# Kernel tuning notes

Hardware: AMD Instinct MI355X
Metric: run time of the kernel (lower is better)

Reference implementation:

```python
import jax, jax.numpy as jnp
import numpy as np

# --- GLIF3 / AlphaPSC constants (from NeuronParam / NetworkConfig) ---
N = 2048            # n_neuron
NE = int(N * 0.8)   # excitatory count = 1638
NUM_IN_NEU = 1024
NUM_OUT_NEU = 128
T, B, NUM_IN, NUM_OUT = 100, 64, 784, 10
V_TH, V_RESET = -45.0, -60.0
C_M, TAU = 2.0, 20.0
K_ASC, ASC_AMP = 1.0 / 80.0, -0.2
TAU_REF, BASE_I = 2.0, 0.12
DT = 1.0


def _spike(x):
    # heaviside spike (Erf surrogate only matters for backward)
    return (x >= 0).astype(x.dtype)


def setup_inputs() -> dict:
    key = jax.random.key(0)
    k1, k2, k3, k4 = jax.random.split(key, 4)
    x = jax.random.normal(k1, (T, B, NUM_IN), jnp.float32)
    W_in = jax.random.normal(k2, (NUM_IN_NEU, NUM_IN), jnp.float32) / np.sqrt(NUM_IN)
    W_rec = jax.random.normal(k3, (N, N), jnp.float32) * (5.0 / np.sqrt(N))  # rec_weight_scaling
    W_out = jax.random.normal(k4, (NUM_OUT, NUM_OUT_NEU), jnp.float32) / np.sqrt(NUM_OUT_NEU)
    # replicate NetworkConfig.__post_init__ index sampling (same RandomState, same order)
    rand = np.random.RandomState(32)
    input_indices = jnp.asarray(rand.choice(NE, NUM_IN_NEU, replace=False), jnp.int32)
    output_indices = jnp.asarray(rand.choice(NE, NUM_OUT_NEU, replace=False), jnp.int32)
    tau_syn = jnp.concatenate([jnp.full((NE,), 5.8, jnp.float32),
                               jnp.full((N - NE,), 6.5, jnp.float32)])
    return dict(x=x, W_in=W_in, W_rec=W_rec, W_out=W_out, tau_syn=tau_syn,
                input_indices=input_indices, output_indices=output_indices)


def _run(x, W_in, W_rec, W_out, tau_syn, input_indices, output_indices, spike_fn):
    Tn, Bn, _ = x.shape
    # input projection then scatter into the excitatory input subset
    proj = jnp.einsum('tbi,ni->tbn', x, W_in)                   # (T, B, num_input_neuron)
    inp = jnp.zeros((Tn, Bn, N), x.dtype).at[..., input_indices].set(proj)
    d_syn = jnp.exp(-DT / tau_syn)                              # (N,) per-neuron alpha decay
    e_tau = jnp.e / tau_syn                                     # alpha-kernel peak normalization
    d_asc = jnp.exp(-K_ASC * DT)

    def step(carry, inp_t):
        v, psc, rise, asc, ref, spk = carry
        # recurrent connection + external drive feeds the alpha synapse
        I_in = spk @ W_rec.T + inp_t                            # (B, N)
        psc_n = d_syn * (psc + DT * rise)                       # alpha-PSC (dual-exp) update
        rise_n = d_syn * rise + e_tau * I_in
        asc_n = d_asc * asc + ASC_AMP * spk                     # after-spike current
        active = (ref <= 0).astype(v.dtype)                     # refractory gate
        dv = (psc_n + asc_n + BASE_I) / C_M - (v - V_RESET) / TAU
        v_n = v + active * DT * dv
        spk_n = spike_fn(v_n - V_TH) * active
        v_n = v_n - spk_n * (V_TH - V_RESET)                    # soft reset (hard_reset=False)
        ref_n = jnp.where(spk_n > 0, TAU_REF, jnp.maximum(ref - DT, 0.0))
        return (v_n, psc_n, rise_n, asc_n, ref_n, spk_n), spk_n

    z = jnp.zeros((Bn, N), x.dtype)
    c0 = (jnp.full((Bn, N), V_RESET, x.dtype), z, z, z, z, z)
    _, spikes = jax.lax.scan(step, c0, inp)                     # spikes: (T, B, N)
    rate = spikes[..., output_indices].mean(axis=0)             # (B, num_output_neuron)
    return rate @ W_out.T                                       # (B, num_output)


def reference(x, W_in, W_rec, W_out, tau_syn, input_indices, output_indices):
    return _run(x, W_in, W_rec, W_out, tau_syn, input_indices, output_indices, _spike)
```

## Files before the change

### kernel.cpp

```cpp
#include <hip/hip_runtime.h>
#include <math.h>

#define N_NEU    2048
#define BB       64
#define TT       100
#define KIN      784
#define NIN_NEU  1024
#define N_OUT    10
#define NOUT_NEU 128

typedef unsigned int u32;
typedef unsigned long long u64;
typedef unsigned short u16;

__global__ void k_prep(const float* __restrict__ tau, double* __restrict__ d_syn,
                       double* __restrict__ e_tau){
    int n = blockIdx.x * blockDim.x + threadIdx.x;
    if(n < N_NEU){
        double tv = (double)tau[n];
        d_syn[n] = exp(-1.0 / tv);
        e_tau[n] = 2.718281828459045 / tv;
    }
}

__global__ void k_zero(double* __restrict__ p, long nels, u64* __restrict__ exch, int nexch){
    long i = (long)blockIdx.x * blockDim.x + threadIdx.x;
    long stride = (long)gridDim.x * blockDim.x;
    for(; i < nels; i += stride) p[i] = 0.0;
    int j = blockIdx.x * blockDim.x + threadIdx.x;
    if(j < nexch) exch[j] = 0ull;
}

__global__ __launch_bounds__(256) void k_tr(const float* __restrict__ Wrec, float* __restrict__ Wt){
    __shared__ float tile[32][33];
    int bx = blockIdx.x, by = blockIdx.y;
    int txx = threadIdx.x, tyy = threadIdx.y;
    #pragma unroll
    for(int j=0;j<4;j++)
        tile[tyy+8*j][txx] = Wrec[(size_t)(by*32 + tyy+8*j)*N_NEU + bx*32 + txx];
    __syncthreads();
    #pragma unroll
    for(int j=0;j<4;j++)
        Wt[(size_t)(bx*32 + tyy+8*j)*N_NEU + by*32 + txx] = tile[txx][tyy+8*j];
}

__global__ __launch_bounds__(256) void k_proj(const float* __restrict__ X, const float* __restrict__ Win,
                                              const int* __restrict__ iidx, double* __restrict__ projG){
    __shared__ float As[32][68];
    __shared__ float Bs[32][68];
    const int r0 = blockIdx.x * 64;
    const int c0 = blockIdx.y * 64;
    const int t  = threadIdx.x;
    const int lr = t >> 2;
    const int lk = (t & 3) * 8;
    const int tx = t & 15, ty = t >> 4;
    double acc[4][4] = {};
    for(int k0 = 0; k0 < KIN; k0 += 32){
        int kk = k0 + lk;
        float a8[8], b8[8];
        if(kk + 8 <= KIN){
            const float* pa = X   + (size_t)(r0+lr)*KIN + kk;
            const float* pb = Win + (size_t)(c0+lr)*KIN + kk;
            float4 ra0 = *reinterpret_cast<const float4*>(pa);
            float4 ra1 = *reinterpret_cast<const float4*>(pa + 4);
            float4 rb0 = *reinterpret_cast<const float4*>(pb);
            float4 rb1 = *reinterpret_cast<const float4*>(pb + 4);
            a8[0]=ra0.x; a8[1]=ra0.y; a8[2]=ra0.z; a8[3]=ra0.w;
            a8[4]=ra1.x; a8[5]=ra1.y; a8[6]=ra1.z; a8[7]=ra1.w;
            b8[0]=rb0.x; b8[1]=rb0.y; b8[2]=rb0.z; b8[3]=rb0.w;
            b8[4]=rb1.x; b8[5]=rb1.y; b8[6]=rb1.z; b8[7]=rb1.w;
        } else {
            #pragma unroll
            for(int e=0;e<8;e++){ a8[e]=0.0f; b8[e]=0.0f; }
        }
        #pragma unroll
        for(int e=0;e<8;e++){ As[lk+e][lr] = a8[e]; Bs[lk+e][lr] = b8[e]; }
        __syncthreads();
        #pragma unroll
        for(int kkk=0;kkk<32;kkk++){
            float4 af = *reinterpret_cast<const float4*>(&As[kkk][ty*4]);
            float4 bf = *reinterpret_cast<const float4*>(&Bs[kkk][tx*4]);
            double a[4] = {(double)af.x,(double)af.y,(double)af.z,(double)af.w};
            double b[4] = {(double)bf.x,(double)bf.y,(double)bf.z,(double)bf.w};
            #pragma unroll
            for(int i=0;i<4;i++)
                #pragma unroll
                for(int j=0;j<4;j++)
                    acc[i][j] += a[i]*b[j];
        }
        __syncthreads();
    }
    const int tt = blockIdx.x;
    #pragma unroll
    for(int j=0;j<4;j++){
        int c = c0 + tx*4 + j;
        int n = iidx[c];
        #pragma unroll
        for(int i=0;i<4;i++){
            int b = ty*4 + i;
            projG[((size_t)b*TT + tt)*N_NEU + n] = acc[i][j];
        }
    }
}

__global__ __launch_bounds__(512) void k_sim(
        const double* __restrict__ projG, const float* __restrict__ Wt,
        const double* __restrict__ dsyn, const double* __restrict__ etau,
        u64* __restrict__ exch, double* __restrict__ cntout){
    __shared__ double Ip[4][512];
    __shared__ u32 words[64];
    __shared__ u16 list[N_NEU];
    __shared__ int cntS;

    const int bid = blockIdx.x;
    const int b   = bid >> 2;
    const int q   = bid & 3;
    const int tid = threadIdx.x;
    const int n   = q*512 + tid;
    const int team = tid >> 7;
    const int c4   = (tid & 127) * 4;
    const float*  WtQ   = Wt + q*512;
    const double* projB = projG + (size_t)b*TT*N_NEU + q*512;

    u64* myE = exch + (size_t)bid*32;

    const double ds = dsyn[n], et = etau[n];
    const double dasc = exp(-0.0125);
    double v=-60.0, psc=0.0, rise=0.0, asc=0.0, ref=0.0, spk=0.0, creg=0.0;

    if(tid == 0) cntS = 0;
    __syncthreads();

    for(int t=0;t<TT;t++){
        double pp = projB[(size_t)t*N_NEU + tid];

        const int cc  = cntS;
        const int beg = (cc * team)     >> 2;
        const int end = (cc * (team+1)) >> 2;
        double I[4] = {0.0, 0.0, 0.0, 0.0};
        int i = beg;
        for(; i + 8 <= end; i += 8){
            int m[8];
            #pragma unroll
            for(int u=0;u<8;u++) m[u] = list[i+u];
            float4 wv[8];
            #pragma unroll
            for(int u=0;u<8;u++)
                wv[u] = *reinterpret_cast<const float4*>(WtQ + ((size_t)m[u] << 11) + c4);
            #pragma unroll
            for(int u=0;u<8;u++){
                I[0] += (double)wv[u].x; I[1] += (double)wv[u].y;
                I[2] += (double)wv[u].z; I[3] += (double)wv[u].w;
            }
        }
        for(; i < end; ++i){
            int mm = list[i];
            float4 w4 = *reinterpret_cast<const float4*>(WtQ + ((size_t)mm << 11) + c4);
            I[0] += (double)w4.x; I[1] += (double)w4.y;
            I[2] += (double)w4.z; I[3] += (double)w4.w;
        }
        #pragma unroll
        for(int u=0;u<4;u++) Ip[team][c4+u] = I[u];
        __syncthreads();

        double Irec = Ip[0][tid] + Ip[1][tid] + Ip[2][tid] + Ip[3][tid] + pp;

        double psc_n  = ds * (psc + rise);
        double rise_n = ds * rise + et * Irec;
        double asc_n  = dasc * asc + (-0.2) * spk;
        double act    = (ref <= 0.0) ? 1.0 : 0.0;
        double dv  = (psc_n + asc_n + 0.12) / 2.0 - (v - (-60.0)) / 20.0;
        double v_n = v + act * dv;
        double s_n = ((v_n - (-45.0)) >= 0.0) ? act : 0.0;
        v_n = v_n - s_n * 15.0;
        double ref_n = (s_n > 0.0) ? 2.0 : fmax(ref - 1.0, 0.0);
        v = v_n; psc = psc_n; rise = rise_n; asc = asc_n; ref = ref_n; spk = s_n;
        creg += s_n;

        u64 bal = __ballot(s_n > 0.0);
        int w = tid >> 6, lane = tid & 63;
        u64 tagv = ((u64)(t+1)) << 32;
        if(lane == 0){
            u32 lo = (u32)bal, hi = (u32)(bal >> 32);
            words[q*16 + 2*w]     = lo;
            words[q*16 + 2*w + 1] = hi;
            u64* dst = myE + (size_t)(t & 1)*16;
            atomicExch(&dst[2*w],     tagv | (u64)lo);
            atomicExch(&dst[2*w + 1], tagv | (u64)hi);
        }
        if(tid < 48){
            int pidx = tid >> 4;
            int w2   = tid & 15;
            int q2   = pidx + (pidx >= q ? 1 : 0);
            u64* src = exch + (size_t)(b*4 + q2)*32 + (size_t)(t & 1)*16;
            u64 val = atomicAdd(&src[w2], 0ull);
            while((val >> 32) != (u64)(t+1)){
                __builtin_amdgcn_s_sleep(1);
                val = atomicAdd(&src[w2], 0ull);
            }
            words[q2*16 + w2] = (u32)val;
        }
        __syncthreads();

        if(tid < 64){
            u32 wv = words[tid];
            int c = __popc(wv);
            int incl = c;
            #pragma unroll
            for(int off=1; off<64; off<<=1){
                int x = __shfl_up(incl, off);
                if(tid >= off) incl += x;
            }
            int excl = incl - c;
            u32 z = wv;
            int base = tid * 32;
            while(z){
                int bp = __ffs(z) - 1;
                z &= z - 1;
                list[excl++] = (u16)(base + bp);
            }
            if(tid == 63) cntS = incl;
        }
        __syncthreads();
    }

    cntout[(size_t)b*N_NEU + n] = creg;
}

__global__ void k_final(const double* __restrict__ cnt, const int* __restrict__ oidx,
                        const float* __restrict__ Wout, float* __restrict__ out){
    int i = blockIdx.x * blockDim.x + threadIdx.x;
    if(i >= BB * N_OUT) return;
    int b = i / N_OUT, o = i - b * N_OUT;
    double accv = 0.0;
    for(int j=0;j<NOUT_NEU;j++){
        double rate = cnt[(size_t)b*N_NEU + oidx[j]] / 100.0;
        accv += rate * (double)Wout[o*NOUT_NEU + j];
    }
    out[i] = (float)accv;
}

extern "C" void kernel_launch(void* const* d_in, const int* in_sizes, int n_in,
                              void* d_out, int out_size, void* d_ws, size_t ws_size,
                              hipStream_t stream){
    const float* X    = (const float*)d_in[0];
    const float* Win  = (const float*)d_in[1];
    const float* Wrec = (const float*)d_in[2];
    const float* Wout = (const float*)d_in[3];
    const float* tau  = (const float*)d_in[4];
    const int*   iidx = (const int*)d_in[5];
    const int*   oidx = (const int*)d_in[6];
    float* out = (float*)d_out;

    char* w = (char*)d_ws;
    const size_t OFF_PROJG = 0;
    const size_t OFF_CNT   = OFF_PROJG + (size_t)BB*TT*N_NEU*8;
    const size_t OFF_WT    = OFF_CNT + (size_t)BB*N_NEU*8;
    const size_t OFF_EXCH  = OFF_WT + (size_t)N_NEU*N_NEU*4;
    const size_t OFF_DS    = OFF_EXCH + 65536;
    const size_t OFF_ET    = OFF_DS + N_NEU*8;

    double* projG = (double*)(w + OFF_PROJG);
    double* cnt   = (double*)(w + OFF_CNT);
    float*  Wt    = (float*)(w + OFF_WT);
    u64*    exch  = (u64*)(w + OFF_EXCH);
    double* dsyn  = (double*)(w + OFF_DS);
    double* etau  = (double*)(w + OFF_ET);

    k_prep <<<dim3(8),      dim3(256),  0, stream>>>(tau, dsyn, etau);
    k_zero <<<dim3(4096),   dim3(256),  0, stream>>>(projG, (long)BB*TT*N_NEU, exch, 8192);
    k_tr   <<<dim3(64,64),  dim3(32,8), 0, stream>>>(Wrec, Wt);
    k_proj <<<dim3(100,16), dim3(256),  0, stream>>>(X, Win, iidx, projG);
    k_sim  <<<dim3(4*BB),   dim3(512),  0, stream>>>(projG, Wt, dsyn, etau, exch, cnt);
    k_final<<<dim3(3),      dim3(256),  0, stream>>>(cnt, oidx, Wout, out);
}
```

Before: 669.7 us.

## Use FP64 MFMA for input projection and store compact projection with inverse index

The input projection GEMM moves from scalar FP64 FMAs to FP64 MFMA instructions. A one-wave probe kernel checks the accumulator layout at runtime and falls back to the VALU kernel if the check fails. The projection is now stored compactly over the 1024 input neurons, and the simulation reads it through an inverse index map, so the large zero-fill of the full scattered buffer is gone. The cost is a few extra tiny launches and one gather per step in the simulation kernel.

```diff
diff --git a/kernel.cpp b/kernel.cpp
--- a/kernel.cpp
+++ b/kernel.cpp
@@ -12,23 +12,52 @@
 typedef unsigned int u32;
 typedef unsigned long long u64;
 typedef unsigned short u16;
+typedef double f64x4 __attribute__((ext_vector_type(4)));
 
 __global__ void k_prep(const float* __restrict__ tau, double* __restrict__ d_syn,
-                       double* __restrict__ e_tau){
+                       double* __restrict__ e_tau, int* __restrict__ inv){
     int n = blockIdx.x * blockDim.x + threadIdx.x;
     if(n < N_NEU){
         double tv = (double)tau[n];
         d_syn[n] = exp(-1.0 / tv);
         e_tau[n] = 2.718281828459045 / tv;
-    }
-}
-
-__global__ void k_zero(double* __restrict__ p, long nels, u64* __restrict__ exch, int nexch){
-    long i = (long)blockIdx.x * blockDim.x + threadIdx.x;
-    long stride = (long)gridDim.x * blockDim.x;
-    for(; i < nels; i += stride) p[i] = 0.0;
+        inv[n] = -1;
+    }
+}
+
+__global__ void k_scatter(const int* __restrict__ idx, int* __restrict__ inv){
+    int j = blockIdx.x * blockDim.x + threadIdx.x;
+    if(j < NIN_NEU) inv[idx[j]] = j;
+}
+
+__global__ void k_zero(u64* __restrict__ exch, int nexch){
     int j = blockIdx.x * blockDim.x + threadIdx.x;
     if(j < nexch) exch[j] = 0ull;
+}
+
+__global__ void k_probe(int* __restrict__ flag){
+    int l = threadIdx.x & 63;
+    double a = (double)((l & 15)*4 + (l >> 4) + 1);
+    double b = (double)((l >> 4)*16 + (l & 15) + 1);
+    f64x4 acc = {0.0, 0.0, 0.0, 0.0};
+    acc = __builtin_amdgcn_mfma_f64_16x16x4f64(a, b, acc, 0, 0, 0);
+    bool oka = true, okb = true;
+    int j = l & 15;
+    #pragma unroll
+    for(int r=0;r<4;r++){
+        int ia = 4*(l >> 4) + r;
+        int ib = (l >> 4) + 4*r;
+        double expA = 0.0, expB = 0.0;
+        #pragma unroll
+        for(int k=0;k<4;k++){
+            expA += (double)((4*ia + k + 1) * (16*k + j + 1));
+            expB += (double)((4*ib + k + 1) * (16*k + j + 1));
+        }
+        oka = oka && (acc[r] == expA);
+        okb = okb && (acc[r] == expB);
+    }
+    bool alla = __all(oka), allb = __all(okb);
+    if(threadIdx.x == 0) *flag = alla ? 0 : (allb ? 1 : 2);
 }
 
 __global__ __launch_bounds__(256) void k_tr(const float* __restrict__ Wrec, float* __restrict__ Wt){
@@ -44,8 +73,72 @@
         Wt[(size_t)(bx*32 + tyy+8*j)*N_NEU + by*32 + txx] = tile[txx][tyy+8*j];
 }
 
-__global__ __launch_bounds__(256) void k_proj(const float* __restrict__ X, const float* __restrict__ Win,
-                                              const int* __restrict__ iidx, double* __restrict__ projG){
+__global__ __launch_bounds__(256) void k_proj_mfma(const float* __restrict__ X, const float* __restrict__ Win,
+                                                   const int* __restrict__ flagp, double* __restrict__ projC){
+    const int flag = *flagp;
+    if(flag >= 2) return;
+    __shared__ float As[32][81];
+    __shared__ float Bs[32][81];
+    const int t   = blockIdx.x;
+    const int c0  = blockIdx.y * 64;
+    const int tid = threadIdx.x;
+    const int w   = tid >> 6;
+    const int l   = tid & 63;
+    const int g   = l >> 4;
+    const int cl  = l & 15;
+    const int lr  = tid >> 2;
+    const int lk  = (tid & 3) * 8;
+
+    f64x4 acc[4] = {{0.,0.,0.,0.},{0.,0.,0.,0.},{0.,0.,0.,0.},{0.,0.,0.,0.}};
+
+    for(int k0 = 0; k0 < KIN; k0 += 32){
+        int kk = k0 + lk;
+        float a8[8], b8[8];
+        if(kk + 8 <= KIN){
+            const float* pa = X   + (size_t)(t*64 + lr)*KIN + kk;
+            const float* pb = Win + (size_t)(c0 + lr)*KIN + kk;
+            float4 ra0 = *reinterpret_cast<const float4*>(pa);
+            float4 ra1 = *reinterpret_cast<const float4*>(pa + 4);
+            float4 rb0 = *reinterpret_cast<const float4*>(pb);
+            float4 rb1 = *reinterpret_cast<const float4*>(pb + 4);
+            a8[0]=ra0.x; a8[1]=ra0.y; a8[2]=ra0.z; a8[3]=ra0.w;
+            a8[4]=ra1.x; a8[5]=ra1.y; a8[6]=ra1.z; a8[7]=ra1.w;
+            b8[0]=rb0.x; b8[1]=rb0.y; b8[2]=rb0.z; b8[3]=rb0.w;
+            b8[4]=rb1.x; b8[5]=rb1.y; b8[6]=rb1.z; b8[7]=rb1.w;
+        } else {
+            #pragma unroll
+            for(int e=0;e<8;e++){ a8[e]=0.0f; b8[e]=0.0f; }
+        }
+        #pragma unroll
+        for(int e=0;e<8;e++){ As[lk+e][lr] = a8[e]; Bs[lk+e][lr] = b8[e]; }
+        __syncthreads();
+
+        #pragma unroll
+        for(int kq=0;kq<8;kq++){
+            double a = (double)As[kq*4 + g][w*16 + cl];
+            #pragma unroll
+            for(int ct=0;ct<4;ct++){
+                double bb = (double)Bs[kq*4 + g][ct*16 + cl];
+                acc[ct] = __builtin_amdgcn_mfma_f64_16x16x4f64(a, bb, acc[ct], 0, 0, 0);
+            }
+        }
+        __syncthreads();
+    }
+
+    #pragma unroll
+    for(int ct=0;ct<4;ct++){
+        int c = c0 + ct*16 + cl;
+        #pragma unroll
+        for(int j=0;j<4;j++){
+            int b = w*16 + ((flag == 0) ? (4*g + j) : (g + 4*j));
+            projC[((size_t)b*TT + t)*NIN_NEU + c] = acc[ct][j];
+        }
+    }
+}
+
+__global__ __launch_bounds__(256) void k_proj_valu(const float* __restrict__ X, const float* __restrict__ Win,
+                                                   const int* __restrict__ flagp, double* __restrict__ projC){
+    if(*flagp < 2) return;
     __shared__ float As[32][68];
     __shared__ float Bs[32][68];
     const int r0 = blockIdx.x * 64;
@@ -94,18 +187,18 @@
     #pragma unroll
     for(int j=0;j<4;j++){
         int c = c0 + tx*4 + j;
-        int n = iidx[c];
         #pragma unroll
         for(int i=0;i<4;i++){
             int b = ty*4 + i;
-            projG[((size_t)b*TT + tt)*N_NEU + n] = acc[i][j];
+            projC[((size_t)b*TT + tt)*NIN_NEU + c] = acc[i][j];
         }
     }
 }
 
 __global__ __launch_bounds__(512) void k_sim(
-        const double* __restrict__ projG, const float* __restrict__ Wt,
+        const double* __restrict__ projC, const float* __restrict__ Wt,
         const double* __restrict__ dsyn, const double* __restrict__ etau,
+        const int* __restrict__ inv,
         u64* __restrict__ exch, double* __restrict__ cntout){
     __shared__ double Ip[4][512];
     __shared__ u32 words[64];
@@ -120,11 +213,12 @@
     const int team = tid >> 7;
     const int c4   = (tid & 127) * 4;
     const float*  WtQ   = Wt + q*512;
-    const double* projB = projG + (size_t)b*TT*N_NEU + q*512;
+    const double* projB = projC + (size_t)b*TT*NIN_NEU;
 
     u64* myE = exch + (size_t)bid*32;
 
     const double ds = dsyn[n], et = etau[n];
+    const int jv = inv[n];
     const double dasc = exp(-0.0125);
     double v=-60.0, psc=0.0, rise=0.0, asc=0.0, ref=0.0, spk=0.0, creg=0.0;
 
@@ -132,7 +226,7 @@
     __syncthreads();
 
     for(int t=0;t<TT;t++){
-        double pp = projB[(size_t)t*N_NEU + tid];
+        double pp = (jv >= 0) ? projB[(size_t)t*NIN_NEU + jv] : 0.0;
 
         const int cc  = cntS;
         const int beg = (cc * team)     >> 2;
@@ -253,24 +347,31 @@
     float* out = (float*)d_out;
 
     char* w = (char*)d_ws;
-    const size_t OFF_PROJG = 0;
-    const size_t OFF_CNT   = OFF_PROJG + (size_t)BB*TT*N_NEU*8;
-    const size_t OFF_WT    = OFF_CNT + (size_t)BB*N_NEU*8;
-    const size_t OFF_EXCH  = OFF_WT + (size_t)N_NEU*N_NEU*4;
-    const size_t OFF_DS    = OFF_EXCH + 65536;
-    const size_t OFF_ET    = OFF_DS + N_NEU*8;
-
-    double* projG = (double*)(w + OFF_PROJG);
+    const size_t OFF_PROJ = 0;
+    const size_t OFF_CNT  = OFF_PROJ + (size_t)BB*TT*NIN_NEU*8;
+    const size_t OFF_WT   = OFF_CNT + (size_t)BB*N_NEU*8;
+    const size_t OFF_EXCH = OFF_WT + (size_t)N_NEU*N_NEU*4;
+    const size_t OFF_DS   = OFF_EXCH + 65536;
+    const size_t OFF_ET   = OFF_DS + N_NEU*8;
+    const size_t OFF_INV  = OFF_ET + N_NEU*8;
+    const size_t OFF_FLAG = OFF_INV + N_NEU*4;
+
+    double* projC = (double*)(w + OFF_PROJ);
     double* cnt   = (double*)(w + OFF_CNT);
     float*  Wt    = (float*)(w + OFF_WT);
     u64*    exch  = (u64*)(w + OFF_EXCH);
     double* dsyn  = (double*)(w + OFF_DS);
     double* etau  = (double*)(w + OFF_ET);
-
-    k_prep <<<dim3(8),      dim3(256),  0, stream>>>(tau, dsyn, etau);
-    k_zero <<<dim3(4096),   dim3(256),  0, stream>>>(projG, (long)BB*TT*N_NEU, exch, 8192);
-    k_tr   <<<dim3(64,64),  dim3(32,8), 0, stream>>>(Wrec, Wt);
-    k_proj <<<dim3(100,16), dim3(256),  0, stream>>>(X, Win, iidx, projG);
-    k_sim  <<<dim3(4*BB),   dim3(512),  0, stream>>>(projG, Wt, dsyn, etau, exch, cnt);
-    k_final<<<dim3(3),      dim3(256),  0, stream>>>(cnt, oidx, Wout, out);
-}
+    int*    inv   = (int*)(w + OFF_INV);
+    int*    flag  = (int*)(w + OFF_FLAG);
+
+    k_prep     <<<dim3(8),      dim3(256),  0, stream>>>(tau, dsyn, etau, inv);
+    k_scatter  <<<dim3(4),      dim3(256),  0, stream>>>(iidx, inv);
+    k_zero     <<<dim3(32),     dim3(256),  0, stream>>>(exch, 8192);
+    k_probe    <<<dim3(1),      dim3(64),   0, stream>>>(flag);
+    k_tr       <<<dim3(64,64),  dim3(32,8), 0, stream>>>(Wrec, Wt);
+    k_proj_mfma<<<dim3(100,16), dim3(256),  0, stream>>>(X, Win, flag, projC);
+    k_proj_valu<<<dim3(100,16), dim3(256),  0, stream>>>(X, Win, flag, projC);
+    k_sim      <<<dim3(4*BB),   dim3(512),  0, stream>>>(projC, Wt, dsyn, etau, inv, exch, cnt);
+    k_final    <<<dim3(3),      dim3(256),  0, stream>>>(cnt, oidx, Wout, out);
+}
```

Measured after the change: 573.5 us. 14.4% less time.
